# Kernel optimization log

Measured on AMD Instinct MI355X. Metric: run time of the kernel, lower is better.

Reference implementation:

```python
import jax, jax.numpy as jnp
import numpy as np
from jax import lax

N_RAYS, N_STEPS, G = 4096, 160, 160
COLOR_DIM, WIDTH = 3, 128
POS_PE, VIEW_PE = 5, 4
XYZ_MIN, XYZ_MAX = -1.0, 1.0
NEAR = 0.05
STEPSIZE = 0.5
VOXEL_SIZE = (XYZ_MAX - XYZ_MIN) / G
DIST = STEPSIZE * VOXEL_SIZE
S_VAL = 80.0
FASTCOLOR_THRES = 1e-7
MASK_THRES = 1e-3
ALPHA_INIT = 1e-4
ACT_SHIFT = float(np.log(1.0 / (1.0 - ALPHA_INIT) - 1.0))
SMOOTH_K, SMOOTH_SIGMA = 5, 1.0
POSFREQ = jnp.asarray([2.0 ** i for i in range(POS_PE)], jnp.float32)
VIEWFREQ = jnp.asarray([2.0 ** i for i in range(VIEW_PE)], jnp.float32)


def _gauss_kernel():
    ax = np.arange(SMOOTH_K) - SMOOTH_K // 2
    g = np.exp(-(ax ** 2) / (2.0 * SMOOTH_SIGMA ** 2))
    k = g[:, None, None] * g[None, :, None] * g[None, None, :]
    return jnp.asarray(k / k.sum(), np.float32)[None, None]


def _trilerp(grid, pts):
    # grid [C,Gx,Gx,Gx]; pts [...,3] in world coords -> [..., C] (align_corners trilinear)
    Gx = grid.shape[-1]
    u = (pts - XYZ_MIN) / (XYZ_MAX - XYZ_MIN) * (Gx - 1)
    u = jnp.clip(u, 0.0, Gx - 1.0)
    i0 = jnp.clip(jnp.floor(u).astype(jnp.int32), 0, Gx - 2)
    f = u - i0.astype(u.dtype)
    x0, y0, z0 = i0[..., 0], i0[..., 1], i0[..., 2]
    fx, fy, fz = f[..., 0], f[..., 1], f[..., 2]
    def g8(ix, iy, iz):
        return grid[:, ix, iy, iz]  # [C, ...]
    out = (g8(x0, y0, z0) * (1 - fx) * (1 - fy) * (1 - fz)
         + g8(x0, y0, z0 + 1) * (1 - fx) * (1 - fy) * fz
         + g8(x0, y0 + 1, z0) * (1 - fx) * fy * (1 - fz)
         + g8(x0, y0 + 1, z0 + 1) * (1 - fx) * fy * fz
         + g8(x0 + 1, y0, z0) * fx * (1 - fy) * (1 - fz)
         + g8(x0 + 1, y0, z0 + 1) * fx * (1 - fy) * fz
         + g8(x0 + 1, y0 + 1, z0) * fx * fy * (1 - fz)
         + g8(x0 + 1, y0 + 1, z0 + 1) * fx * fy * fz)
    return jnp.moveaxis(out, 0, -1)


def _alphas2weights(alpha):
    # per-ray (segmented) exclusive cumprod of transmittance; alpha [N,S]
    T = jnp.cumprod(1.0 - alpha, axis=1)
    T_excl = jnp.concatenate([jnp.ones_like(T[:, :1]), T[:, :-1]], axis=1)
    return alpha * T_excl, T[:, -1]


def _mlp(x, w0, b0, w1, b1, w2, b2):
    h = jax.nn.relu(x @ w0 + b0)
    h = jax.nn.relu(h @ w1 + b1)
    return h @ w2 + b2


def _forward(rays_o, rays_d, viewdirs, sdf_grid, mask_density,
             off_color_grid, emo_color_grid,
             off_w0, off_b0, off_w1, off_b1, off_w2, off_b2,
             emo_w0, emo_b0, emo_w1, emo_b1, emo_w2, emo_b2, em_modes):
    N = rays_o.shape[0]
    t = NEAR + DIST * jnp.arange(N_STEPS, dtype=jnp.float32)
    ray_pts = rays_o[:, None, :] + rays_d[:, None, :] * t[None, :, None]  # [N,S,3]

    # MaskCache: threshold alpha from coarse density grid (boolean keep mask)
    dens = _trilerp(mask_density, ray_pts)[..., 0]
    mask_alpha = 1.0 - jnp.exp(-jax.nn.softplus(dens + ACT_SHIFT) * DIST)
    keep0 = mask_alpha >= MASK_THRES  # [N,S]

    # Gaussian-smoothed SDF grid + central-difference gradient grid
    sdf_s = lax.conv_general_dilated(sdf_grid, _gauss_kernel(), (1, 1, 1), 'SAME',
                                     dimension_numbers=('NCDHW', 'OIDHW', 'NCDHW'))[0]  # [1,G,G,G]
    s = sdf_s[0]
    grad_grid = jnp.zeros((3, G, G, G), sdf_grid.dtype)
    grad_grid = grad_grid.at[0, 1:-1].set((s[2:] - s[:-2]) / (2 * VOXEL_SIZE))
    grad_grid = grad_grid.at[1, :, 1:-1].set((s[:, 2:] - s[:, :-2]) / (2 * VOXEL_SIZE))
    grad_grid = grad_grid.at[2, :, :, 1:-1].set((s[:, :, 2:] - s[:, :, :-2]) / (2 * VOXEL_SIZE))

    sdf = _trilerp(sdf_s, ray_pts)[..., 0]   # [N,S]
    gradient = _trilerp(grad_grid, ray_pts)  # [N,S,3]

    # NeuS alpha from sdf (scatter, grad variant, cos_anneal = 1)
    true_cos = jnp.einsum('nd,nsd->ns', viewdirs, gradient)
    iter_cos = -jax.nn.relu(-true_cos)
    prev_cdf = jax.nn.sigmoid((sdf - iter_cos * DIST * 0.5) * S_VAL)
    next_cdf = jax.nn.sigmoid((sdf + iter_cos * DIST * 0.5) * S_VAL)
    alpha = jnp.clip((prev_cdf - next_cdf + 1e-5) / (prev_cdf + 1e-5), 0.0, 1.0)
    alpha = jnp.where(keep0, alpha, 0.0)  # masked points contribute nothing

    weights, _ = _alphas2weights(alpha)
    keep1 = weights > FASTCOLOR_THRES
    alpha = jnp.where(keep1, alpha, 0.0)
    weights, alphainv_last = _alphas2weights(alpha)

    # features: pos PE, view PE (per-ray, gathered by ray_id == broadcast), normal
    rays_xyz = (ray_pts - XYZ_MIN) / (XYZ_MAX - XYZ_MIN)  # [N,S,3]
    xyz_emb = (rays_xyz[..., None] * POSFREQ).reshape(N, N_STEPS, -1)
    v_emb = (viewdirs[..., None] * VIEWFREQ).reshape(N, -1)
    v_full = jnp.concatenate([v_emb, jnp.sin(v_emb), jnp.cos(v_emb)], -1)
    v_full = jnp.broadcast_to(v_full[:, None, :], (N, N_STEPS, v_full.shape[-1]))
    normal = gradient / (jnp.linalg.norm(gradient, axis=-1, keepdims=True) + 1e-5)
    rgb_feat = jnp.concatenate([rays_xyz, jnp.sin(xyz_emb), jnp.cos(xyz_emb), v_full, normal], -1)

    off_in = jnp.concatenate([_trilerp(off_color_grid, ray_pts), rgb_feat], -1)
    emo_in = jnp.concatenate([_trilerp(emo_color_grid, ray_pts), rgb_feat], -1)
    off_rgb = jax.nn.sigmoid(_mlp(off_in, off_w0, off_b0, off_w1, off_b1, off_w2, off_b2))
    emo_rgb = jax.nn.sigmoid(_mlp(emo_in, emo_w0, emo_b0, emo_w1, emo_b1, emo_w2, emo_b2))
    on_mask = (em_modes == 1)[:, None, None]  # em_modes[ray_id] == 1
    rgb = jnp.where(on_mask, emo_rgb, 0.0) + off_rgb

    w_ = weights[..., None]
    rgb_marched = jnp.sum(w_ * rgb, axis=1)  # segment_coo(sum over ray_id)
    cum_weights = jnp.sum(w_, axis=1)        # [N,1]
    return rgb_marched, alphainv_last, 1.0 - cum_weights


def setup_inputs() -> dict:
    key = jax.random.key(0)
    ks = jax.random.split(key, 12)
    rays_o = jax.random.uniform(ks[0], (N_RAYS, 3), jnp.float32, -0.3, 0.3)
    rd = jax.random.normal(ks[1], (N_RAYS, 3), jnp.float32)
    rays_d = rd / jnp.linalg.norm(rd, axis=-1, keepdims=True)
    viewdirs = rays_d
    em_modes = jax.random.randint(ks[2], (N_RAYS,), 0, 2)
    lin = np.linspace(-1.0, 1.0, G, dtype=np.float32)
    x, y, z = np.meshgrid(lin, lin, lin, indexing='ij')
    sdf_grid = jnp.asarray(np.sqrt(x ** 2 + y ** 2 + z ** 2) - 1.0)[None, None]  # sphere-SDF init
    mask_density = jax.random.normal(ks[3], (1, 80, 80, 80), jnp.float32) * 2.0 + 12.0
    off_color_grid = jax.random.normal(ks[4], (COLOR_DIM, G, G, G), jnp.float32) * 0.1
    emo_color_grid = jax.random.normal(ks[5], (COLOR_DIM, G, G, G), jnp.float32) * 0.1
    DIM0 = 3 + 3 * POS_PE * 2 + 3 * VIEW_PE * 3 + COLOR_DIM + 3  # = 75
    def lw(k, i, o):
        return jax.random.normal(k, (i, o), jnp.float32) * (1.0 / np.sqrt(i))
    return dict(rays_o=rays_o, rays_d=rays_d, viewdirs=viewdirs, em_modes=em_modes,
                sdf_grid=sdf_grid, mask_density=mask_density,
                off_color_grid=off_color_grid, emo_color_grid=emo_color_grid,
                off_w0=lw(ks[6], DIM0, WIDTH), off_b0=jnp.zeros((WIDTH,), jnp.float32),
                off_w1=lw(ks[7], WIDTH, WIDTH), off_b1=jnp.zeros((WIDTH,), jnp.float32),
                off_w2=lw(ks[8], WIDTH, 3), off_b2=jnp.zeros((3,), jnp.float32),
                emo_w0=lw(ks[9], DIM0, WIDTH), emo_b0=jnp.zeros((WIDTH,), jnp.float32),
                emo_w1=lw(ks[10], WIDTH, WIDTH), emo_b1=jnp.zeros((WIDTH,), jnp.float32),
                emo_w2=lw(ks[11], WIDTH, 3), emo_b2=jnp.zeros((3,), jnp.float32))


def reference(rays_o, rays_d, viewdirs, em_modes, sdf_grid, mask_density,
              off_color_grid, emo_color_grid,
              off_w0, off_b0, off_w1, off_b1, off_w2, off_b2,
              emo_w0, emo_b0, emo_w1, emo_b1, emo_w2, emo_b2):
    return _forward(rays_o, rays_d, viewdirs, sdf_grid, mask_density,
                    off_color_grid, emo_color_grid,
                    off_w0, off_b0, off_w1, off_b1, off_w2, off_b2,
                    emo_w0, emo_b0, emo_w1, emo_b1, emo_w2, emo_b2, em_modes)
```

## Files before the change

### kernel.cpp

```cpp
#include <hip/hip_runtime.h>

#define NRAYS 4096
#define NSTEPS 160
#define NSAMP (NRAYS*NSTEPS)
#define GG 160
#define GG2 (GG*GG)
#define GG3 (GG*GG2)
#define GM 80
#define GM2 (GM*GM)

#define NEARV 0.05f
#define DISTV 0.00625f
#define SVAL 80.0f
#define ACT_SHIFT_C (-9.2102403669758813f)
#define INV2H 40.0f
#define MASK_THRES_C 1e-3f
#define FAST_THRES_C 1e-7f

#define KW0 0.05448868454964295f
#define KW1 0.24420134200323332f
#define KW2 0.40261994689424750f

__device__ __forceinline__ float sigmf(float x){ return 1.0f/(1.0f+__expf(-x)); }
__device__ __forceinline__ float softplusf_(float x){ return (x>20.0f)? x : log1pf(__expf(x)); }

__device__ __forceinline__ void tricoord(float p, int Gx, int& i0, float& fr){
  float u = (p + 1.0f)*0.5f*(float)(Gx-1);
  u = fminf(fmaxf(u, 0.0f), (float)(Gx-1));
  int i = (int)floorf(u);
  i = min(max(i,0), Gx-2);
  i0 = i; fr = u - (float)i;
}

__global__ __launch_bounds__(256) void ksmooth_yz(const float* __restrict__ in, float* __restrict__ out,
                                                  float* __restrict__ outbuf, int* __restrict__ cnt){
  __shared__ float S[36][37];
  __shared__ float Tz[36][33];
  const int bx = blockIdx.x;
  const int t = threadIdx.x;
  if (bx == 0){
    for (int i = t; i < NRAYS*3; i += 256) outbuf[i] = 0.0f;
    if (t < 2) cnt[t] = 0;
  }
  const int x  = bx / 25;
  const int tile = bx % 25;
  const int Y0 = (tile/5)*32, Z0 = (tile%5)*32;
  const float kw[5] = {KW0,KW1,KW2,KW1,KW0};
  for (int i = t; i < 36*36; i += 256){
    int r = i/36, c = i - (i/36)*36;
    int y = Y0 + r - 2, z = Z0 + c - 2;
    float v = 0.0f;
    if (y>=0 && y<GG && z>=0 && z<GG) v = in[(x*GG+y)*GG+z];
    S[r][c] = v;
  }
  __syncthreads();
  for (int i = t; i < 36*32; i += 256){
    int r = i >> 5, c = i & 31;
    float acc = 0.f;
    #pragma unroll
    for (int d=0; d<5; d++) acc += kw[d]*S[r][c+d];
    Tz[r][c] = acc;
  }
  __syncthreads();
  for (int i = t; i < 32*32; i += 256){
    int yy = i >> 5, c = i & 31;
    float acc = 0.f;
    #pragma unroll
    for (int d=0; d<5; d++) acc += kw[d]*Tz[yy+d][c];
    out[(x*GG + Y0+yy)*GG + Z0 + c] = acc;
  }
}

__global__ __launch_bounds__(64) void kmarch(
  const float* __restrict__ ro, const float* __restrict__ rd,
  const float* __restrict__ vd, const int* __restrict__ em,
  const float* __restrict__ maskg, const float* __restrict__ Y,
  int* __restrict__ slist, float* __restrict__ sw, float* __restrict__ sgrad,
  int* __restrict__ cnt, float* __restrict__ out)
{
  int n = blockIdx.x*64 + threadIdx.x;
  if (n >= NRAYS) return;
  const float ox=ro[n*3+0], oy=ro[n*3+1], oz=ro[n*3+2];
  const float dx=rd[n*3+0], dy=rd[n*3+1], dz=rd[n*3+2];
  const float vx=vd[n*3+0], vy=vd[n*3+1], vz=vd[n*3+2];
  const int emn = em[n];
  const float kwc[5] = {KW0,KW1,KW2,KW1,KW0};
  float T1=1.0f, T2=1.0f, cum=0.0f;
  for (int s=0; s<NSTEPS; s++){
    float tt = NEARV + DISTV*(float)s;
    float px = ox + dx*tt, py = oy + dy*tt, pz = oz + dz*tt;

    int mx,my,mz; float mfx,mfy,mfz;
    tricoord(px, GM, mx, mfx); tricoord(py, GM, my, mfy); tricoord(pz, GM, mz, mfz);
    int mid = (mx*GM + my)*GM + mz;
    float d000=maskg[mid],        d001=maskg[mid+1];
    float d010=maskg[mid+GM],     d011=maskg[mid+GM+1];
    float d100=maskg[mid+GM2],    d101=maskg[mid+GM2+1];
    float d110=maskg[mid+GM2+GM], d111=maskg[mid+GM2+GM+1];
    float m00 = d000 + (d001-d000)*mfz;
    float m01 = d010 + (d011-d010)*mfz;
    float m10 = d100 + (d101-d100)*mfz;
    float m11 = d110 + (d111-d110)*mfz;
    float m0 = m00 + (m01-m00)*mfy;
    float m1 = m10 + (m11-m10)*mfy;
    float dens = m0 + (m1-m0)*mfx;
    float malpha = 1.0f - __expf(-softplusf_(dens + ACT_SHIFT_C)*DISTV);

    int ix,iy,iz; float fx,fy,fz;
    tricoord(px, GG, ix, fx); tricoord(py, GG, iy, fy); tricoord(pz, GG, iz, fz);

    float R[2][2][8];
    #pragma unroll
    for (int jb=0;jb<2;jb++)
      #pragma unroll
      for (int jc=0;jc<2;jc++)
        #pragma unroll
        for (int j=0;j<8;j++){
          int a = ix-3+j;
          R[jb][jc][j] = (a>=0 && a<GG) ? Y[(a*GG + iy+jb)*GG + iz+jc] : 0.0f;
        }
    const bool hasym = (iy>=1), hasyp = (iy<=GG-3);
    const bool haszm = (iz>=1), haszp = (iz<=GG-3);
    float Eym[2][6], Eyp[2][6], Ezm[2][6], Ezp[2][6];
    #pragma unroll
    for (int jc=0;jc<2;jc++)
      #pragma unroll
      for (int j=0;j<6;j++){
        int a = ix-2+j;
        bool ax = (a>=0 && a<GG);
        Eym[jc][j] = (hasym && ax) ? Y[(a*GG + iy-1)*GG + iz+jc] : 0.0f;
        Eyp[jc][j] = (hasyp && ax) ? Y[(a*GG + iy+2)*GG + iz+jc] : 0.0f;
      }
    #pragma unroll
    for (int jb=0;jb<2;jb++)
      #pragma unroll
      for (int j=0;j<6;j++){
        int a = ix-2+j;
        bool ax = (a>=0 && a<GG);
        Ezm[jb][j] = (haszm && ax) ? Y[(a*GG + iy+jb)*GG + iz-1] : 0.0f;
        Ezp[jb][j] = (haszp && ax) ? Y[(a*GG + iy+jb)*GG + iz+2] : 0.0f;
      }

    float sdf=0.0f, gx=0.0f, gy=0.0f, gz=0.0f;
    #pragma unroll
    for (int ja=0;ja<2;ja++){
      #pragma unroll
      for (int jb=0;jb<2;jb++){
        #pragma unroll
        for (int jc=0;jc<2;jc++){
          float w = (ja?fx:1.0f-fx)*(jb?fy:1.0f-fy)*(jc?fz:1.0f-fz);
          const float* r = R[jb][jc];
          float s0=0.0f;
          #pragma unroll
          for (int t2=0;t2<5;t2++) s0 += kwc[t2]*r[ja+1+t2];
          sdf += w*s0;
          int a = ix+ja, b = iy+jb, c = iz+jc;
          if (a>=1 && a<=GG-2){
            float sp=0.0f, sm=0.0f;
            #pragma unroll
            for (int t2=0;t2<5;t2++){ sp += kwc[t2]*r[ja+2+t2]; sm += kwc[t2]*r[ja+t2]; }
            gx += w*INV2H*(sp-sm);
          }
          if (b>=1 && b<=GG-2){
            float acc=0.0f;
            if (jb==0){
              const float* up = R[1][jc];
              const float* dn = Eym[jc];
              #pragma unroll
              for (int t2=0;t2<5;t2++) acc += kwc[t2]*(up[ja+1+t2] - dn[ja+t2]);
            } else {
              const float* up = Eyp[jc];
              const float* dn = R[0][jc];
              #pragma unroll
              for (int t2=0;t2<5;t2++) acc += kwc[t2]*(up[ja+t2] - dn[ja+1+t2]);
            }
            gy += w*INV2H*acc;
          }
          if (c>=1 && c<=GG-2){
            float acc=0.0f;
            if (jc==0){
              const float* up = R[jb][1];
              const float* dn = Ezm[jb];
              #pragma unroll
              for (int t2=0;t2<5;t2++) acc += kwc[t2]*(up[ja+1+t2] - dn[ja+t2]);
            } else {
              const float* up = Ezp[jb];
              const float* dn = R[jb][0];
              #pragma unroll
              for (int t2=0;t2<5;t2++) acc += kwc[t2]*(up[ja+t2] - dn[ja+1+t2]);
            }
            gz += w*INV2H*acc;
          }
        }
      }
    }

    float tc = vx*gx + vy*gy + vz*gz;
    float icos = fminf(tc, 0.0f);
    float e = icos*DISTV*0.5f;
    float prev = sigmf((sdf - e)*SVAL);
    float nxt  = sigmf((sdf + e)*SVAL);
    float alpha = (prev - nxt + 1e-5f)/(prev + 1e-5f);
    alpha = fminf(fmaxf(alpha, 0.0f), 1.0f);
    if (!(malpha >= MASK_THRES_C)) alpha = 0.0f;

    float w1 = alpha*T1; T1 *= (1.0f - alpha);
    float a2 = (w1 > FAST_THRES_C) ? alpha : 0.0f;
    float wv = a2*T2;   T2 *= (1.0f - a2);
    cum += wv;
    if (wv > 0.0f){
      int pos;
      if (emn == 1){ int p = atomicAdd(&cnt[1], 1); pos = NSAMP - 1 - p; }
      else         { pos = atomicAdd(&cnt[0], 1); }
      slist[pos] = n*NSTEPS + s;
      sw[pos] = wv;
      sgrad[pos*3+0]=gx; sgrad[pos*3+1]=gy; sgrad[pos*3+2]=gz;
    }
    if (T1 <= FAST_THRES_C) break;
  }
  out[NRAYS*3 + n] = T2;
  out[NRAYS*4 + n] = 1.0f - cum;
}

__global__ __launch_bounds__(256) void kmlp6(
  const float* __restrict__ ro, const float* __restrict__ rd,
  const float* __restrict__ vd,
  const float* __restrict__ offc, const float* __restrict__ emoc,
  const int* __restrict__ slist, const float* __restrict__ sw,
  const float* __restrict__ sgrad, const int* __restrict__ cnt,
  const float* __restrict__ W0o, const float* __restrict__ b0o,
  const float* __restrict__ W1o, const float* __restrict__ b1o,
  const float* __restrict__ W2o, const float* __restrict__ b2o,
  const float* __restrict__ W0e, const float* __restrict__ b0e,
  const float* __restrict__ W1e, const float* __restrict__ b1e,
  const float* __restrict__ W2e, const float* __restrict__ b2e,
  float* __restrict__ out)
{
  __shared__ float X[16][80];
  __shared__ float H[16][132];
  __shared__ float H2[16][132];
  __shared__ float OUTB[16][3];
  __shared__ float WSH[16];
  __shared__ float GS[16][3];
  __shared__ int SSAMP[16];

  const int t = threadIdx.x;
  const int c0 = cnt[0];
  const int c1 = cnt[1];
  const int head = blockIdx.x & 1;
  const int cstride = gridDim.x >> 1;
  const int total = head ? c1 : (c0 + c1);
  const int seg1 = NSAMP - c1;

  const float* W0 = head ? W0e : W0o;  const float* b0 = head ? b0e : b0o;
  const float* W1 = head ? W1e : W1o;  const float* b1 = head ? b1e : b1o;
  const float* W2 = head ? W2e : W2o;  const float* b2 = head ? b2e : b2o;
  const float* cg = head ? emoc : offc;
  const float4* W04 = (const float4*)W0;
  const float4* W14 = (const float4*)W1;

  const int lane = t & 31;
  const int sg   = t >> 5;

  for (int chunk = blockIdx.x >> 1; chunk*16 < total; chunk += cstride) {
    const int base = chunk*16;
    if (t < 16) {
      int v = base + t;
      bool vld = (v < total);
      int i;
      if (head) i = seg1 + v;
      else      i = (v < c0) ? v : seg1 + (v - c0);
      if (!vld) i = head ? seg1 : 0;
      int samp = vld ? slist[i] : 0;
      SSAMP[t] = samp;
      WSH[t]   = vld ? sw[i] : 0.0f;
      GS[t][0] = vld ? sgrad[i*3+0] : 0.0f;
      GS[t][1] = vld ? sgrad[i*3+1] : 0.0f;
      GS[t][2] = vld ? sgrad[i*3+2] : 0.0f;
    }
    __syncthreads();

    {
      const int s = t & 15;
      const int r = t >> 4;
      const int samp = SSAMP[s];
      const int n = samp / NSTEPS;
      const int step = samp - n*NSTEPS;
      const float tt = NEARV + DISTV*(float)step;
      const float px = ro[n*3+0] + rd[n*3+0]*tt;
      const float py = ro[n*3+1] + rd[n*3+1]*tt;
      const float pz = ro[n*3+2] + rd[n*3+2]*tt;
      if (r < 3) {
        int ix,iy,iz; float fx,fy,fz;
        tricoord(px, GG, ix, fx); tricoord(py, GG, iy, fy); tricoord(pz, GG, iz, fz);
        const float* g = cg + (size_t)r * GG3;
        const int id = (ix*GG + iy)*GG + iz;
        float v000=g[id],        v001=g[id+1];
        float v010=g[id+GG],     v011=g[id+GG+1];
        float v100=g[id+GG2],    v101=g[id+GG2+1];
        float v110=g[id+GG2+GG], v111=g[id+GG2+GG+1];
        float c00 = v000 + (v001-v000)*fz;
        float c01 = v010 + (v011-v010)*fz;
        float c10 = v100 + (v101-v100)*fz;
        float c11 = v110 + (v111-v110)*fz;
        float cl0 = c00 + (c01-c00)*fy;
        float cl1 = c10 + (c11-c10)*fy;
        X[s][r] = cl0 + (cl1-cl0)*fx;
      } else if (r == 3) {
        X[s][3] = (px+1.0f)*0.5f;
        X[s][4] = (py+1.0f)*0.5f;
        X[s][5] = (pz+1.0f)*0.5f;
        float gx = GS[s][0], gy = GS[s][1], gz = GS[s][2];
        float inv = 1.0f/(sqrtf(gx*gx+gy*gy+gz*gz)+1e-5f);
        X[s][72] = gx*inv; X[s][73] = gy*inv; X[s][74] = gz*inv;
        X[s][75] = 0.0f; X[s][76] = 0.0f; X[s][77] = 0.0f; X[s][78] = 0.0f; X[s][79] = 0.0f;
      } else if (r < 7) {
        const int a = r - 4;
        const float coord = (a==0)?px:((a==1)?py:pz);
        const float rxyz = (coord+1.0f)*0.5f;
        float fr = 1.0f;
        #pragma unroll
        for (int q = 0; q < 5; q++) {
          float e = rxyz*fr; fr *= 2.0f;
          X[s][6  + a*5 + q] = __sinf(e);
          X[s][21 + a*5 + q] = __cosf(e);
        }
      } else if (r < 10) {
        const int a = r - 7;
        const int n2 = SSAMP[s] / NSTEPS;
        const float v = vd[n2*3+a];
        float fr = 1.0f;
        #pragma unroll
        for (int q = 0; q < 4; q++) {
          float e = v*fr; fr *= 2.0f;
          X[s][36 + a*4 + q] = e;
          X[s][48 + a*4 + q] = __sinf(e);
          X[s][60 + a*4 + q] = __cosf(e);
        }
      }
    }
    __syncthreads();

    {
      const float4 bb = ((const float4*)b0)[lane];
      float4 a0 = bb, a1 = bb;
      const int s0 = sg*2;
      #pragma unroll 3
      for (int k4 = 0; k4 < 72; k4 += 4){
        float4 w0 = W04[(k4+0)*32 + lane];
        float4 w1 = W04[(k4+1)*32 + lane];
        float4 w2 = W04[(k4+2)*32 + lane];
        float4 w3 = W04[(k4+3)*32 + lane];
        float4 x0 = *(const float4*)&X[s0+0][k4];
        float4 x1 = *(const float4*)&X[s0+1][k4];
        a0.x+=x0.x*w0.x; a0.y+=x0.x*w0.y; a0.z+=x0.x*w0.z; a0.w+=x0.x*w0.w;
        a1.x+=x1.x*w0.x; a1.y+=x1.x*w0.y; a1.z+=x1.x*w0.z; a1.w+=x1.x*w0.w;
        a0.x+=x0.y*w1.x; a0.y+=x0.y*w1.y; a0.z+=x0.y*w1.z; a0.w+=x0.y*w1.w;
        a1.x+=x1.y*w1.x; a1.y+=x1.y*w1.y; a1.z+=x1.y*w1.z; a1.w+=x1.y*w1.w;
        a0.x+=x0.z*w2.x; a0.y+=x0.z*w2.y; a0.z+=x0.z*w2.z; a0.w+=x0.z*w2.w;
        a1.x+=x1.z*w2.x; a1.y+=x1.z*w2.y; a1.z+=x1.z*w2.z; a1.w+=x1.z*w2.w;
        a0.x+=x0.w*w3.x; a0.y+=x0.w*w3.y; a0.z+=x0.w*w3.z; a0.w+=x0.w*w3.w;
        a1.x+=x1.w*w3.x; a1.y+=x1.w*w3.y; a1.z+=x1.w*w3.z; a1.w+=x1.w*w3.w;
      }
      #pragma unroll
      for (int k = 72; k < 75; k++){
        float4 w = W04[k*32 + lane];
        float x0 = X[s0+0][k], x1 = X[s0+1][k];
        a0.x+=x0*w.x; a0.y+=x0*w.y; a0.z+=x0*w.z; a0.w+=x0*w.w;
        a1.x+=x1*w.x; a1.y+=x1*w.y; a1.z+=x1*w.z; a1.w+=x1*w.w;
      }
      H[s0+0][lane*4+0]=fmaxf(a0.x,0.f); H[s0+0][lane*4+1]=fmaxf(a0.y,0.f);
      H[s0+0][lane*4+2]=fmaxf(a0.z,0.f); H[s0+0][lane*4+3]=fmaxf(a0.w,0.f);
      H[s0+1][lane*4+0]=fmaxf(a1.x,0.f); H[s0+1][lane*4+1]=fmaxf(a1.y,0.f);
      H[s0+1][lane*4+2]=fmaxf(a1.z,0.f); H[s0+1][lane*4+3]=fmaxf(a1.w,0.f);
    }
    __syncthreads();

    {
      const float4 bb = ((const float4*)b1)[lane];
      float4 a0 = bb, a1 = bb;
      const int s0 = sg*2;
      #pragma unroll 4
      for (int k4 = 0; k4 < 128; k4 += 4){
        float4 w0 = W14[(k4+0)*32 + lane];
        float4 w1 = W14[(k4+1)*32 + lane];
        float4 w2 = W14[(k4+2)*32 + lane];
        float4 w3 = W14[(k4+3)*32 + lane];
        float4 x0 = *(const float4*)&H[s0+0][k4];
        float4 x1 = *(const float4*)&H[s0+1][k4];
        a0.x+=x0.x*w0.x; a0.y+=x0.x*w0.y; a0.z+=x0.x*w0.z; a0.w+=x0.x*w0.w;
        a1.x+=x1.x*w0.x; a1.y+=x1.x*w0.y; a1.z+=x1.x*w0.z; a1.w+=x1.x*w0.w;
        a0.x+=x0.y*w1.x; a0.y+=x0.y*w1.y; a0.z+=x0.y*w1.z; a0.w+=x0.y*w1.w;
        a1.x+=x1.y*w1.x; a1.y+=x1.y*w1.y; a1.z+=x1.y*w1.z; a1.w+=x1.y*w1.w;
        a0.x+=x0.z*w2.x; a0.y+=x0.z*w2.y; a0.z+=x0.z*w2.z; a0.w+=x0.z*w2.w;
        a1.x+=x1.z*w2.x; a1.y+=x1.z*w2.y; a1.z+=x1.z*w2.z; a1.w+=x1.z*w2.w;
        a0.x+=x0.w*w3.x; a0.y+=x0.w*w3.y; a0.z+=x0.w*w3.z; a0.w+=x0.w*w3.w;
        a1.x+=x1.w*w3.x; a1.y+=x1.w*w3.y; a1.z+=x1.w*w3.z; a1.w+=x1.w*w3.w;
      }
      H2[s0+0][lane*4+0]=fmaxf(a0.x,0.f); H2[s0+0][lane*4+1]=fmaxf(a0.y,0.f);
      H2[s0+0][lane*4+2]=fmaxf(a0.z,0.f); H2[s0+0][lane*4+3]=fmaxf(a0.w,0.f);
      H2[s0+1][lane*4+0]=fmaxf(a1.x,0.f); H2[s0+1][lane*4+1]=fmaxf(a1.y,0.f);
      H2[s0+1][lane*4+2]=fmaxf(a1.z,0.f); H2[s0+1][lane*4+3]=fmaxf(a1.w,0.f);
    }
    __syncthreads();

    {
      const int s0 = sg*2;
      #pragma unroll
      for (int i = 0; i < 2; i++){
        const int s = s0 + i;
        float4 h = *(const float4*)&H2[s][lane*4];
        float c0v = h.x*W2[(lane*4+0)*3+0] + h.y*W2[(lane*4+1)*3+0]
                  + h.z*W2[(lane*4+2)*3+0] + h.w*W2[(lane*4+3)*3+0];
        float c1v = h.x*W2[(lane*4+0)*3+1] + h.y*W2[(lane*4+1)*3+1]
                  + h.z*W2[(lane*4+2)*3+1] + h.w*W2[(lane*4+3)*3+1];
        float c2v = h.x*W2[(lane*4+0)*3+2] + h.y*W2[(lane*4+1)*3+2]
                  + h.z*W2[(lane*4+2)*3+2] + h.w*W2[(lane*4+3)*3+2];
        #pragma unroll
        for (int d=16; d>=1; d>>=1){
          c0v += __shfl_down(c0v, d, 32);
          c1v += __shfl_down(c1v, d, 32);
          c2v += __shfl_down(c2v, d, 32);
        }
        if (lane == 0){
          OUTB[s][0] = sigmf(c0v + b2[0]);
          OUTB[s][1] = sigmf(c1v + b2[1]);
          OUTB[s][2] = sigmf(c2v + b2[2]);
        }
      }
    }
    __syncthreads();

    if (t < 48) {
      int s2 = t/3, c = t - s2*3;
      float w = WSH[s2];
      if (w > 0.0f) {
        int n2 = SSAMP[s2]/NSTEPS;
        atomicAdd(&out[n2*3 + c], w * OUTB[s2][c]);
      }
    }
    __syncthreads();
  }
}

extern "C" void kernel_launch(void* const* d_in, const int* in_sizes, int n_in,
                              void* d_out, int out_size, void* d_ws, size_t ws_size,
                              hipStream_t stream) {
  const float* ro    = (const float*)d_in[0];
  const float* rd    = (const float*)d_in[1];
  const float* vd    = (const float*)d_in[2];
  const int*   em    = (const int*)d_in[3];
  const float* sdfg  = (const float*)d_in[4];
  const float* maskg = (const float*)d_in[5];
  const float* offc  = (const float*)d_in[6];
  const float* emoc  = (const float*)d_in[7];
  const float* W0o = (const float*)d_in[8];
  const float* b0o = (const float*)d_in[9];
  const float* W1o = (const float*)d_in[10];
  const float* b1o = (const float*)d_in[11];
  const float* W2o = (const float*)d_in[12];
  const float* b2o = (const float*)d_in[13];
  const float* W0e = (const float*)d_in[14];
  const float* b0e = (const float*)d_in[15];
  const float* W1e = (const float*)d_in[16];
  const float* b1e = (const float*)d_in[17];
  const float* W2e = (const float*)d_in[18];
  const float* b2e = (const float*)d_in[19];

  float* out = (float*)d_out;
  float* ws  = (float*)d_ws;
  float* Yb    = ws;
  float* swb   = ws + GG3;
  float* sgradb= swb + NSAMP;
  int*   slist = (int*)(sgradb + 3*(size_t)NSAMP);
  int*   cnt   = slist + NSAMP;

  ksmooth_yz<<<GG*25, 256, 0, stream>>>(sdfg, Yb, out, cnt);

  kmarch<<<NRAYS/64, 64, 0, stream>>>(ro, rd, vd, em, maskg, Yb,
                                      slist, swb, sgradb, cnt, out);

  kmlp6<<<1024, 256, 0, stream>>>(ro, rd, vd, offc, emoc,
                                  slist, swb, sgradb, cnt,
                                  W0o,b0o,W1o,b1o,W2o,b2o,
                                  W0e,b0e,W1e,b1e,W2e,b2e, out);
}
```

Baseline: 56.20 us.

## Restructure MLP kernel to per-wavefront sample pairs without block barriers

```diff
diff --git a/kernel.cpp b/kernel.cpp
--- a/kernel.cpp
+++ b/kernel.cpp
@@ -222,7 +222,7 @@
   out[NRAYS*4 + n] = 1.0f - cum;
 }
 
-__global__ __launch_bounds__(256) void kmlp6(
+__global__ __launch_bounds__(256) void kmlp7(
   const float* __restrict__ ro, const float* __restrict__ rd,
   const float* __restrict__ vd,
   const float* __restrict__ offc, const float* __restrict__ emoc,
@@ -236,54 +236,49 @@
   const float* __restrict__ W2e, const float* __restrict__ b2e,
   float* __restrict__ out)
 {
-  __shared__ float X[16][80];
-  __shared__ float H[16][132];
-  __shared__ float H2[16][132];
-  __shared__ float OUTB[16][3];
-  __shared__ float WSH[16];
-  __shared__ float GS[16][3];
-  __shared__ int SSAMP[16];
+  __shared__ float X[4][2][80];
+  __shared__ float H[4][2][128];
 
   const int t = threadIdx.x;
-  const int c0 = cnt[0];
-  const int c1 = cnt[1];
-  const int head = blockIdx.x & 1;
-  const int cstride = gridDim.x >> 1;
-  const int total = head ? c1 : (c0 + c1);
+  const int wid = t >> 6;
+  const int lt  = t & 63;
+  const int c0 = cnt[0], c1 = cnt[1];
   const int seg1 = NSAMP - c1;
-
-  const float* W0 = head ? W0e : W0o;  const float* b0 = head ? b0e : b0o;
-  const float* W1 = head ? W1e : W1o;  const float* b1 = head ? b1e : b1o;
-  const float* W2 = head ? W2e : W2o;  const float* b2 = head ? b2e : b2o;
-  const float* cg = head ? emoc : offc;
-  const float4* W04 = (const float4*)W0;
-  const float4* W14 = (const float4*)W1;
-
-  const int lane = t & 31;
-  const int sg   = t >> 5;
-
-  for (int chunk = blockIdx.x >> 1; chunk*16 < total; chunk += cstride) {
-    const int base = chunk*16;
-    if (t < 16) {
-      int v = base + t;
-      bool vld = (v < total);
-      int i;
-      if (head) i = seg1 + v;
-      else      i = (v < c0) ? v : seg1 + (v - c0);
-      if (!vld) i = head ? seg1 : 0;
-      int samp = vld ? slist[i] : 0;
-      SSAMP[t] = samp;
-      WSH[t]   = vld ? sw[i] : 0.0f;
-      GS[t][0] = vld ? sgrad[i*3+0] : 0.0f;
-      GS[t][1] = vld ? sgrad[i*3+1] : 0.0f;
-      GS[t][2] = vld ? sgrad[i*3+2] : 0.0f;
-    }
-    __syncthreads();
-
+  const int totOff = c0 + c1;
+  const int nOff = (totOff + 1) >> 1;
+  const int nEmo = (c1 + 1) >> 1;
+  const int nTask = nOff + nEmo;
+
+  for (int task = blockIdx.x*4 + wid; task < nTask; task += gridDim.x*4) {
+    const int head = (task >= nOff) ? 1 : 0;
+    const int total = head ? c1 : totOff;
+    const int v0 = (head ? (task - nOff) : task) * 2;
+
+    const float* W0 = head ? W0e : W0o;  const float* b0 = head ? b0e : b0o;
+    const float* W1 = head ? W1e : W1o;  const float* b1 = head ? b1e : b1o;
+    const float* W2 = head ? W2e : W2o;  const float* b2 = head ? b2e : b2o;
+    const float* cg = head ? emoc : offc;
+    const float4* W04 = (const float4*)W0;
+    const float4* W14 = (const float4*)W1;
+
+    int my_i; float my_w; int my_samp;
     {
-      const int s = t & 15;
-      const int r = t >> 4;
-      const int samp = SSAMP[s];
+      int v = v0 + (lt & 1);
+      int vc = (v < total) ? v : (total - 1);
+      int i = head ? (seg1 + vc) : ((vc < c0) ? vc : seg1 + (vc - c0));
+      my_i = i;
+      my_samp = slist[i];
+      my_w = (v < total) ? sw[i] : 0.0f;
+    }
+    const int iA = __shfl(my_i, 0, 64),    iB = __shfl(my_i, 1, 64);
+    const int sampA = __shfl(my_samp, 0, 64), sampB = __shfl(my_samp, 1, 64);
+    const float wgtA = __shfl(my_w, 0, 64),   wgtB = __shfl(my_w, 1, 64);
+
+    {
+      const int s = lt & 1;
+      const int r = lt >> 1;
+      const int samp = s ? sampB : sampA;
+      const int gi   = s ? iB : iA;
       const int n = samp / NSTEPS;
       const int step = samp - n*NSTEPS;
       const float tt = NEARV + DISTV*(float)step;
@@ -305,15 +300,16 @@
         float c11 = v110 + (v111-v110)*fz;
         float cl0 = c00 + (c01-c00)*fy;
         float cl1 = c10 + (c11-c10)*fy;
-        X[s][r] = cl0 + (cl1-cl0)*fx;
+        X[wid][s][r] = cl0 + (cl1-cl0)*fx;
       } else if (r == 3) {
-        X[s][3] = (px+1.0f)*0.5f;
-        X[s][4] = (py+1.0f)*0.5f;
-        X[s][5] = (pz+1.0f)*0.5f;
-        float gx = GS[s][0], gy = GS[s][1], gz = GS[s][2];
+        X[wid][s][3] = (px+1.0f)*0.5f;
+        X[wid][s][4] = (py+1.0f)*0.5f;
+        X[wid][s][5] = (pz+1.0f)*0.5f;
+        float gx = sgrad[gi*3+0], gy = sgrad[gi*3+1], gz = sgrad[gi*3+2];
         float inv = 1.0f/(sqrtf(gx*gx+gy*gy+gz*gz)+1e-5f);
-        X[s][72] = gx*inv; X[s][73] = gy*inv; X[s][74] = gz*inv;
-        X[s][75] = 0.0f; X[s][76] = 0.0f; X[s][77] = 0.0f; X[s][78] = 0.0f; X[s][79] = 0.0f;
+        X[wid][s][72] = gx*inv; X[wid][s][73] = gy*inv; X[wid][s][74] = gz*inv;
+        X[wid][s][75] = 0.0f; X[wid][s][76] = 0.0f;
+        X[wid][s][77] = 0.0f; X[wid][s][78] = 0.0f; X[wid][s][79] = 0.0f;
       } else if (r < 7) {
         const int a = r - 4;
         const float coord = (a==0)?px:((a==1)?py:pz);
@@ -322,124 +318,94 @@
         #pragma unroll
         for (int q = 0; q < 5; q++) {
           float e = rxyz*fr; fr *= 2.0f;
-          X[s][6  + a*5 + q] = __sinf(e);
-          X[s][21 + a*5 + q] = __cosf(e);
+          X[wid][s][6  + a*5 + q] = __sinf(e);
+          X[wid][s][21 + a*5 + q] = __cosf(e);
         }
       } else if (r < 10) {
         const int a = r - 7;
-        const int n2 = SSAMP[s] / NSTEPS;
-        const float v = vd[n2*3+a];
+        const float v = vd[n*3+a];
         float fr = 1.0f;
         #pragma unroll
         for (int q = 0; q < 4; q++) {
           float e = v*fr; fr *= 2.0f;
-          X[s][36 + a*4 + q] = e;
-          X[s][48 + a*4 + q] = __sinf(e);
-          X[s][60 + a*4 + q] = __cosf(e);
+          X[wid][s][36 + a*4 + q] = e;
+          X[wid][s][48 + a*4 + q] = __sinf(e);
+          X[wid][s][60 + a*4 + q] = __cosf(e);
         }
       }
     }
-    __syncthreads();
-
+
+    const int sme = lt >> 5;
+    const int l32 = lt & 31;
+    const float* Xs = X[wid][sme];
+    const float myw = sme ? wgtB : wgtA;
+    const int mysamp = sme ? sampB : sampA;
+
+    float4 h4;
     {
-      const float4 bb = ((const float4*)b0)[lane];
-      float4 a0 = bb, a1 = bb;
-      const int s0 = sg*2;
+      float4 acc = ((const float4*)b0)[l32];
       #pragma unroll 3
       for (int k4 = 0; k4 < 72; k4 += 4){
-        float4 w0 = W04[(k4+0)*32 + lane];
-        float4 w1 = W04[(k4+1)*32 + lane];
-        float4 w2 = W04[(k4+2)*32 + lane];
-        float4 w3 = W04[(k4+3)*32 + lane];
-        float4 x0 = *(const float4*)&X[s0+0][k4];
-        float4 x1 = *(const float4*)&X[s0+1][k4];
-        a0.x+=x0.x*w0.x; a0.y+=x0.x*w0.y; a0.z+=x0.x*w0.z; a0.w+=x0.x*w0.w;
-        a1.x+=x1.x*w0.x; a1.y+=x1.x*w0.y; a1.z+=x1.x*w0.z; a1.w+=x1.x*w0.w;
-        a0.x+=x0.y*w1.x; a0.y+=x0.y*w1.y; a0.z+=x0.y*w1.z; a0.w+=x0.y*w1.w;
-        a1.x+=x1.y*w1.x; a1.y+=x1.y*w1.y; a1.z+=x1.y*w1.z; a1.w+=x1.y*w1.w;
-        a0.x+=x0.z*w2.x; a0.y+=x0.z*w2.y; a0.z+=x0.z*w2.z; a0.w+=x0.z*w2.w;
-        a1.x+=x1.z*w2.x; a1.y+=x1.z*w2.y; a1.z+=x1.z*w2.z; a1.w+=x1.z*w2.w;
-        a0.x+=x0.w*w3.x; a0.y+=x0.w*w3.y; a0.z+=x0.w*w3.z; a0.w+=x0.w*w3.w;
-        a1.x+=x1.w*w3.x; a1.y+=x1.w*w3.y; a1.z+=x1.w*w3.z; a1.w+=x1.w*w3.w;
+        float4 w0 = W04[(k4+0)*32 + l32];
+        float4 w1 = W04[(k4+1)*32 + l32];
+        float4 w2 = W04[(k4+2)*32 + l32];
+        float4 w3 = W04[(k4+3)*32 + l32];
+        float4 x = *(const float4*)&Xs[k4];
+        acc.x+=x.x*w0.x; acc.y+=x.x*w0.y; acc.z+=x.x*w0.z; acc.w+=x.x*w0.w;
+        acc.x+=x.y*w1.x; acc.y+=x.y*w1.y; acc.z+=x.y*w1.z; acc.w+=x.y*w1.w;
+        acc.x+=x.z*w2.x; acc.y+=x.z*w2.y; acc.z+=x.z*w2.z; acc.w+=x.z*w2.w;
+        acc.x+=x.w*w3.x; acc.y+=x.w*w3.y; acc.z+=x.w*w3.z; acc.w+=x.w*w3.w;
       }
       #pragma unroll
       for (int k = 72; k < 75; k++){
-        float4 w = W04[k*32 + lane];
-        float x0 = X[s0+0][k], x1 = X[s0+1][k];
-        a0.x+=x0*w.x; a0.y+=x0*w.y; a0.z+=x0*w.z; a0.w+=x0*w.w;
-        a1.x+=x1*w.x; a1.y+=x1*w.y; a1.z+=x1*w.z; a1.w+=x1*w.w;
-      }
-      H[s0+0][lane*4+0]=fmaxf(a0.x,0.f); H[s0+0][lane*4+1]=fmaxf(a0.y,0.f);
-      H[s0+0][lane*4+2]=fmaxf(a0.z,0.f); H[s0+0][lane*4+3]=fmaxf(a0.w,0.f);
-      H[s0+1][lane*4+0]=fmaxf(a1.x,0.f); H[s0+1][lane*4+1]=fmaxf(a1.y,0.f);
-      H[s0+1][lane*4+2]=fmaxf(a1.z,0.f); H[s0+1][lane*4+3]=fmaxf(a1.w,0.f);
-    }
-    __syncthreads();
+        float4 w = W04[k*32 + l32];
+        float x = Xs[k];
+        acc.x+=x*w.x; acc.y+=x*w.y; acc.z+=x*w.z; acc.w+=x*w.w;
+      }
+      h4.x = fmaxf(acc.x,0.f); h4.y = fmaxf(acc.y,0.f);
+      h4.z = fmaxf(acc.z,0.f); h4.w = fmaxf(acc.w,0.f);
+      *(float4*)&H[wid][sme][l32*4] = h4;
+    }
 
     {
-      const float4 bb = ((const float4*)b1)[lane];
-      float4 a0 = bb, a1 = bb;
-      const int s0 = sg*2;
+      const float* Hs = H[wid][sme];
+      float4 acc = ((const float4*)b1)[l32];
       #pragma unroll 4
       for (int k4 = 0; k4 < 128; k4 += 4){
-        float4 w0 = W14[(k4+0)*32 + lane];
-        float4 w1 = W14[(k4+1)*32 + lane];
-        float4 w2 = W14[(k4+2)*32 + lane];
-        float4 w3 = W14[(k4+3)*32 + lane];
-        float4 x0 = *(const float4*)&H[s0+0][k4];
-        float4 x1 = *(const float4*)&H[s0+1][k4];
-        a0.x+=x0.x*w0.x; a0.y+=x0.x*w0.y; a0.z+=x0.x*w0.z; a0.w+=x0.x*w0.w;
-        a1.x+=x1.x*w0.x; a1.y+=x1.x*w0.y; a1.z+=x1.x*w0.z; a1.w+=x1.x*w0.w;
-        a0.x+=x0.y*w1.x; a0.y+=x0.y*w1.y; a0.z+=x0.y*w1.z; a0.w+=x0.y*w1.w;
-        a1.x+=x1.y*w1.x; a1.y+=x1.y*w1.y; a1.z+=x1.y*w1.z; a1.w+=x1.y*w1.w;
-        a0.x+=x0.z*w2.x; a0.y+=x0.z*w2.y; a0.z+=x0.z*w2.z; a0.w+=x0.z*w2.w;
-        a1.x+=x1.z*w2.x; a1.y+=x1.z*w2.y; a1.z+=x1.z*w2.z; a1.w+=x1.z*w2.w;
-        a0.x+=x0.w*w3.x; a0.y+=x0.w*w3.y; a0.z+=x0.w*w3.z; a0.w+=x0.w*w3.w;
-        a1.x+=x1.w*w3.x; a1.y+=x1.w*w3.y; a1.z+=x1.w*w3.z; a1.w+=x1.w*w3.w;
-      }
-      H2[s0+0][lane*4+0]=fmaxf(a0.x,0.f); H2[s0+0][lane*4+1]=fmaxf(a0.y,0.f);
-      H2[s0+0][lane*4+2]=fmaxf(a0.z,0.f); H2[s0+0][lane*4+3]=fmaxf(a0.w,0.f);
-      H2[s0+1][lane*4+0]=fmaxf(a1.x,0.f); H2[s0+1][lane*4+1]=fmaxf(a1.y,0.f);
-      H2[s0+1][lane*4+2]=fmaxf(a1.z,0.f); H2[s0+1][lane*4+3]=fmaxf(a1.w,0.f);
-    }
-    __syncthreads();
+        float4 w0 = W14[(k4+0)*32 + l32];
+        float4 w1 = W14[(k4+1)*32 + l32];
+        float4 w2 = W14[(k4+2)*32 + l32];
+        float4 w3 = W14[(k4+3)*32 + l32];
+        float4 x = *(const float4*)&Hs[k4];
+        acc.x+=x.x*w0.x; acc.y+=x.x*w0.y; acc.z+=x.x*w0.z; acc.w+=x.x*w0.w;
+        acc.x+=x.y*w1.x; acc.y+=x.y*w1.y; acc.z+=x.y*w1.z; acc.w+=x.y*w1.w;
+        acc.x+=x.z*w2.x; acc.y+=x.z*w2.y; acc.z+=x.z*w2.z; acc.w+=x.z*w2.w;
+        acc.x+=x.w*w3.x; acc.y+=x.w*w3.y; acc.z+=x.w*w3.z; acc.w+=x.w*w3.w;
+      }
+      h4.x = fmaxf(acc.x,0.f); h4.y = fmaxf(acc.y,0.f);
+      h4.z = fmaxf(acc.z,0.f); h4.w = fmaxf(acc.w,0.f);
+    }
 
     {
-      const int s0 = sg*2;
-      #pragma unroll
-      for (int i = 0; i < 2; i++){
-        const int s = s0 + i;
-        float4 h = *(const float4*)&H2[s][lane*4];
-        float c0v = h.x*W2[(lane*4+0)*3+0] + h.y*W2[(lane*4+1)*3+0]
-                  + h.z*W2[(lane*4+2)*3+0] + h.w*W2[(lane*4+3)*3+0];
-        float c1v = h.x*W2[(lane*4+0)*3+1] + h.y*W2[(lane*4+1)*3+1]
-                  + h.z*W2[(lane*4+2)*3+1] + h.w*W2[(lane*4+3)*3+1];
-        float c2v = h.x*W2[(lane*4+0)*3+2] + h.y*W2[(lane*4+1)*3+2]
-                  + h.z*W2[(lane*4+2)*3+2] + h.w*W2[(lane*4+3)*3+2];
-        #pragma unroll
-        for (int d=16; d>=1; d>>=1){
-          c0v += __shfl_down(c0v, d, 32);
-          c1v += __shfl_down(c1v, d, 32);
-          c2v += __shfl_down(c2v, d, 32);
-        }
-        if (lane == 0){
-          OUTB[s][0] = sigmf(c0v + b2[0]);
-          OUTB[s][1] = sigmf(c1v + b2[1]);
-          OUTB[s][2] = sigmf(c2v + b2[2]);
-        }
-      }
-    }
-    __syncthreads();
-
-    if (t < 48) {
-      int s2 = t/3, c = t - s2*3;
-      float w = WSH[s2];
-      if (w > 0.0f) {
-        int n2 = SSAMP[s2]/NSTEPS;
-        atomicAdd(&out[n2*3 + c], w * OUTB[s2][c]);
-      }
-    }
-    __syncthreads();
+      float c0v = h4.x*W2[(l32*4+0)*3+0] + h4.y*W2[(l32*4+1)*3+0]
+                + h4.z*W2[(l32*4+2)*3+0] + h4.w*W2[(l32*4+3)*3+0];
+      float c1v = h4.x*W2[(l32*4+0)*3+1] + h4.y*W2[(l32*4+1)*3+1]
+                + h4.z*W2[(l32*4+2)*3+1] + h4.w*W2[(l32*4+3)*3+1];
+      float c2v = h4.x*W2[(l32*4+0)*3+2] + h4.y*W2[(l32*4+1)*3+2]
+                + h4.z*W2[(l32*4+2)*3+2] + h4.w*W2[(l32*4+3)*3+2];
+      #pragma unroll
+      for (int d=16; d>=1; d>>=1){
+        c0v += __shfl_down(c0v, d, 32);
+        c1v += __shfl_down(c1v, d, 32);
+        c2v += __shfl_down(c2v, d, 32);
+      }
+      if (l32 == 0 && myw > 0.0f){
+        int n2 = mysamp / NSTEPS;
+        atomicAdd(&out[n2*3+0], myw * sigmf(c0v + b2[0]));
+        atomicAdd(&out[n2*3+1], myw * sigmf(c1v + b2[1]));
+        atomicAdd(&out[n2*3+2], myw * sigmf(c2v + b2[2]));
+      }
+    }
   }
 }
 
@@ -480,7 +446,7 @@
   kmarch<<<NRAYS/64, 64, 0, stream>>>(ro, rd, vd, em, maskg, Yb,
                                       slist, swb, sgradb, cnt, out);
 
-  kmlp6<<<1024, 256, 0, stream>>>(ro, rd, vd, offc, emoc,
+  kmlp7<<<1024, 256, 0, stream>>>(ro, rd, vd, offc, emoc,
                                   slist, swb, sgradb, cnt,
                                   W0o,b0o,W1o,b1o,W2o,b2o,
                                   W0e,b0e,W1e,b1e,W2e,b2e, out);
```

Result: slower. 60.66 us (+7.9%).
